# Optimization experiments

Measured on AMD Instinct MI355X. Metric: run time of the kernel, lower is better.

The kernel has to match this reference:

```python
import jax, jax.numpy as jnp
import numpy as np

B, S, D = 4, 2048, 512
H, DK, DV = 8, 64, 64


def setup_inputs() -> dict:
    key = jax.random.key(0)
    ks = jax.random.split(key, 12)
    inv = 1.0 / np.sqrt(D)
    return {
        "query": jax.random.normal(ks[0], (B, S, D), dtype=jnp.float32),
        "value": jax.random.normal(ks[1], (B, S, D), dtype=jnp.float32),
        "attention_mask": jax.random.randint(ks[2], (B, S), 0, 2, dtype=jnp.int32),
        "Wq": jax.random.normal(ks[3], (D, H * DK), dtype=jnp.float32) * inv,
        "bq": jnp.zeros((H * DK,), dtype=jnp.float32),
        "Wk": jax.random.normal(ks[4], (D, H * DK), dtype=jnp.float32) * inv,
        "bk": jnp.zeros((H * DK,), dtype=jnp.float32),
        "Wv": jax.random.normal(ks[5], (D, H * DV), dtype=jnp.float32) * inv,
        "bv": jnp.zeros((H * DV,), dtype=jnp.float32),
        "Wo": jax.random.normal(ks[6], (H * DV, D), dtype=jnp.float32) * inv,
        "bo": jnp.zeros((D,), dtype=jnp.float32),
    }


def _split_heads(x, h):
    b, s, _ = x.shape
    return x.reshape(b, s, h, -1).transpose(0, 2, 1, 3)  # (B,H,S,dh)


def reference(query, value, attention_mask, Wq, bq, Wk, bk, Wv, bv, Wo, bo):
    # QKV projections (activation=None -> identity); key defaults to value
    q = _split_heads(query @ Wq + bq, H)   # (B,H,S,DK)
    k = _split_heads(value @ Wk + bk, H)   # (B,H,S,DK)
    v = _split_heads(value @ Wv + bv, H)   # (B,H,S,DV)

    scores = jnp.einsum("bhqd,bhkd->bhqk", q, k) / jnp.sqrt(jnp.float32(DK))
    # additive mask: m = 1e9*(mask-1), applied on both key and query axes
    m = 1e9 * (attention_mask.astype(jnp.float32) - 1.0)  # (B,S)
    scores = scores + m[:, None, None, :] + m[:, None, :, None]

    weights = jax.nn.softmax(scores, axis=-1)
    ctx = jnp.einsum("bhqk,bhkd->bhqd", weights, v)        # (B,H,S,DV)
    ctx = ctx.transpose(0, 2, 1, 3).reshape(ctx.shape[0], ctx.shape[2], H * DV)
    return ctx @ Wo + bo  # (B,S,D)
```

## Files before the change

### kernel.cpp

```cpp
#include <hip/hip_runtime.h>

#define B_ 4
#define S_ 2048
#define D_ 512
#define H_ 8

typedef __attribute__((ext_vector_type(8))) __bf16 bf16x8;
typedef __attribute__((ext_vector_type(4))) float f32x4;

#define NEGBIG  -1.442695040e9f
#define QSCALE  0.18033688011112042f

__device__ __forceinline__ unsigned pack_rn(float a, float b) {
    union { float f; unsigned u; } ua, ub; ua.f = a; ub.f = b;
    return __builtin_amdgcn_perm(ub.u + 0x8000u, ua.u + 0x8000u, 0x07060302u);
}

__device__ __forceinline__ void gl16(const void* g, void* l) {
    __builtin_amdgcn_global_load_lds(
        (const __attribute__((address_space(1))) unsigned int*)g,
        (__attribute__((address_space(3))) unsigned int*)l, 16, 0, 0);
}

__global__ __launch_bounds__(256) void pre_all(
    const float* __restrict__ q, const float* __restrict__ v,
    const int* __restrict__ am,
    const float* __restrict__ Wq, const float* __restrict__ Wk,
    const float* __restrict__ Wv, const float* __restrict__ Wo,
    unsigned short* __restrict__ xq, unsigned short* __restrict__ xv,
    unsigned short* __restrict__ Tq, unsigned short* __restrict__ Tk,
    unsigned short* __restrict__ Tv, unsigned short* __restrict__ To,
    int* __restrict__ idxc, int* __restrict__ nvout,
    float* __restrict__ Mf, float* __restrict__ Mc)
{
    const int bid = blockIdx.x;
    const int tid = threadIdx.x;

    if (bid < 4096) {
        const int z = bid >> 11, xb = bid & 2047;
        const float* src = z ? v : q;
        unsigned short* dst = z ? xv : xq;
        int i = (xb * 256 + tid) * 8;
        float4 f0 = *(const float4*)&src[i];
        float4 f1 = *(const float4*)&src[i + 4];
        uint4 o;
        o.x = pack_rn(f0.x, f0.y); o.y = pack_rn(f0.z, f0.w);
        o.z = pack_rn(f1.x, f1.y); o.w = pack_rn(f1.z, f1.w);
        *(uint4*)&dst[i] = o;
    } else if (bid < 4352) {
        int r = bid - 4096;
        int z = r >> 6, rem = r & 63;
        const float* W = (z == 0) ? Wq : (z == 1) ? Wk : (z == 2) ? Wv : Wo;
        unsigned short* T = (z == 0) ? Tq : (z == 1) ? Tk : (z == 2) ? Tv : To;
        int n0 = (rem & 7) * 64, k0 = (rem >> 3) * 64;

        __shared__ float Ts[64][69];
        #pragma unroll
        for (int it = 0; it < 4; it++) {
            int lin = tid + it * 256;
            int kr = lin >> 4, c4 = (lin & 15) * 4;
            float4 vv = *(const float4*)&W[(k0 + kr) * 512 + n0 + c4];
            Ts[kr][c4 + 0] = vv.x; Ts[kr][c4 + 1] = vv.y;
            Ts[kr][c4 + 2] = vv.z; Ts[kr][c4 + 3] = vv.w;
        }
        __syncthreads();
        int n = tid >> 2, kc = tid & 3;
        unsigned p[8];
        #pragma unroll
        for (int j = 0; j < 8; j++)
            p[j] = pack_rn(Ts[kc * 16 + 2 * j][n], Ts[kc * 16 + 2 * j + 1][n]);
        unsigned short* dst = &T[(n0 + n) * 512 + k0 + kc * 16];
        *(uint4*)dst       = *(uint4*)&p[0];
        *(uint4*)(dst + 8) = *(uint4*)&p[4];
    } else {
        const int w = tid >> 6, lane = tid & 63;
        const int* amb = am + w * 2048;
        int m[32];
        #pragma unroll
        for (int s = 0; s < 32; s++) m[s] = amb[s * 64 + lane];

        int* ib = idxc + w * 2048;
        const unsigned long long lt = (1ULL << lane) - 1ULL;
        int base = 0;
        #pragma unroll
        for (int s = 0; s < 32; s++) {
            unsigned long long bal = __ballot(m[s] != 0);
            if (m[s]) ib[base + __popcll(bal & lt)] = s * 64 + lane;
            base += __popcll(bal);
        }
        const int nv = base;
        for (int i = nv + lane; i < 2048; i += 64) ib[i] = 0;
        float* mfb = Mf + w * 2048;
        float* mcb = Mc + w * 2048;
        #pragma unroll
        for (int s = 0; s < 32; s++) {
            int i = s * 64 + lane;
            mfb[i] = m[s] ? 0.f : NEGBIG;
            mcb[i] = (i < nv) ? 0.f : NEGBIG;
        }
        if (lane == 0) nvout[w] = nv;
    }
}

__global__ __launch_bounds__(256) void proj_qkv_mfma(
    const unsigned short* __restrict__ Xq, const unsigned short* __restrict__ Xv,
    const unsigned short* __restrict__ Wtq, const unsigned short* __restrict__ Wtk,
    const unsigned short* __restrict__ Wtv,
    const float* __restrict__ bq, const float* __restrict__ bk,
    const float* __restrict__ bv,
    const int* __restrict__ idxc, const int* __restrict__ nv1,
    unsigned short* __restrict__ Qb, unsigned short* __restrict__ Kb,
    unsigned short* __restrict__ VtG)
{
    const int z = blockIdx.z;
    const unsigned short* A  = (z == 0) ? Wtq : (z == 1) ? Wtk : Xv;
    const unsigned short* Bm = (z == 0) ? Xq  : (z == 1) ? Xv  : Wtv;
    const float* bias        = (z == 0) ? bq  : (z == 1) ? bk  : bv;
    const int lin0 = blockIdx.y * 128 + blockIdx.x;
    const int m0 = (z < 2) ? blockIdx.y * 128 : (lin0 >> 3) * 128;
    const int n0 = (z < 2) ? blockIdx.x * 64  : (lin0 & 7) * 64;

    if (z == 1) {
        int bb = n0 >> 11, cap = (nv1[bb] + 63) & ~63;
        if (cap < 64) cap = 64;
        if ((n0 & 2047) >= cap) return;
    }
    if (z == 2) {
        int bb = m0 >> 11, cap = (nv1[bb] + 63) & ~63;
        if (cap < 64) cap = 64;
        if ((m0 & 2047) >= cap) return;
    }

    const int tid = threadIdx.x;
    const int w = tid >> 6, lane = tid & 63;
    const int l15 = lane & 15, quad = lane >> 4;
    const int wm = (w >> 1) * 64, wn = (w & 1) * 32;

    __shared__ unsigned short As[2][128 * 64];
    __shared__ unsigned short Bs[2][64 * 64];

    const int srw  = tid >> 3;
    const int csrc = (tid & 7) ^ (srw & 7);
    const unsigned short* aS[4];
    const unsigned short* bS[2];
    #pragma unroll
    for (int is = 0; is < 4; is++) {
        int ra = m0 + is * 32 + srw;
        long sa = ra;
        if (z == 2) { int bb = ra >> 11; sa = (long)bb * 2048 + idxc[bb * 2048 + (ra & 2047)]; }
        aS[is] = A + sa * 512 + csrc * 8;
    }
    #pragma unroll
    for (int is = 0; is < 2; is++) {
        int rb = n0 + is * 32 + srw;
        long sb = rb;
        if (z == 1) { int bb = rb >> 11; sb = (long)bb * 2048 + idxc[bb * 2048 + (rb & 2047)]; }
        bS[is] = Bm + sb * 512 + csrc * 8;
    }

    const int koff0 = ((quad    ) ^ (l15 & 7)) * 8;
    const int koff1 = ((quad + 4) ^ (l15 & 7)) * 8;

    f32x4 acc[4][2];
    #pragma unroll
    for (int i = 0; i < 4; i++)
        #pragma unroll
        for (int j = 0; j < 2; j++) acc[i][j] = (f32x4){0.f, 0.f, 0.f, 0.f};

    #define STAGE_Q(buf, k0)                                        \
        do {                                                        \
            _Pragma("unroll")                                       \
            for (int is = 0; is < 4; is++)                          \
                gl16(aS[is] + (k0), &As[buf][is * 2048 + w * 512]); \
            _Pragma("unroll")                                       \
            for (int is = 0; is < 2; is++)                          \
                gl16(bS[is] + (k0), &Bs[buf][is * 2048 + w * 512]); \
        } while (0)

    STAGE_Q(0, 0);
    for (int k = 0; k < 8; k++) {
        const int cur = k & 1;
        if (k < 7) {
            STAGE_Q(cur ^ 1, (k + 1) * 64);
            asm volatile("s_waitcnt vmcnt(6)" ::: "memory");
        } else {
            asm volatile("s_waitcnt vmcnt(0)" ::: "memory");
        }
        asm volatile("s_barrier" ::: "memory");
        #pragma unroll
        for (int kc = 0; kc < 2; kc++) {
            const int ko = kc ? koff1 : koff0;
            bf16x8 a[4], bb[2];
            #pragma unroll
            for (int i = 0; i < 4; i++)
                a[i] = *(const bf16x8*)&As[cur][(wm + 16 * i + l15) * 64 + ko];
            #pragma unroll
            for (int j = 0; j < 2; j++)
                bb[j] = *(const bf16x8*)&Bs[cur][(wn + 16 * j + l15) * 64 + ko];
            #pragma unroll
            for (int i = 0; i < 4; i++)
                #pragma unroll
                for (int j = 0; j < 2; j++)
                    acc[i][j] = __builtin_amdgcn_mfma_f32_16x16x32_bf16(a[i], bb[j], acc[i][j], 0, 0, 0);
        }
        asm volatile("s_barrier" ::: "memory");
    }
    #undef STAGE_Q

    if (z == 2) {
        #pragma unroll
        for (int j = 0; j < 2; j++) {
            int N = n0 + wn + 16 * j + l15;
            float bv_ = bias[N];
            int h = N >> 6, d = N & 63;
            #pragma unroll
            for (int i = 0; i < 4; i++) {
                int Mb = m0 + wm + 16 * i + quad * 4;
                int b = Mb >> 11, s = Mb & 2047;
                uint2 o;
                o.x = pack_rn(acc[i][j][0] + bv_, acc[i][j][1] + bv_);
                o.y = pack_rn(acc[i][j][2] + bv_, acc[i][j][3] + bv_);
                *(uint2*)&VtG[((b * H_ + h) * 64 + d) * 2048 + s] = o;
            }
        }
    } else {
        unsigned short* dst = (z == 0) ? Qb : Kb;
        const float scale = (z == 0) ? QSCALE : 1.0f;
        #pragma unroll
        for (int j = 0; j < 2; j++) {
            int sg = n0 + wn + 16 * j + l15;
            int b = sg >> 11, s = sg & 2047;
            #pragma unroll
            for (int i = 0; i < 4; i++) {
                int F = m0 + wm + 16 * i + quad * 4;
                int h = F >> 6, d = F & 63;
                float4 b4 = *(const float4*)&bias[F];
                uint2 o;
                o.x = pack_rn((acc[i][j][0] + b4.x) * scale, (acc[i][j][1] + b4.y) * scale);
                o.y = pack_rn((acc[i][j][2] + b4.z) * scale, (acc[i][j][3] + b4.w) * scale);
                *(uint2*)&dst[((b * H_ + h) * 2048 + s) * 64 + d] = o;
            }
        }
    }
}

__global__ __launch_bounds__(256, 2) void flash_mfma(
    const unsigned short* __restrict__ Qg, const unsigned short* __restrict__ Kg,
    const unsigned short* __restrict__ VtG, const float* __restrict__ Mf,
    const float* __restrict__ Mc, const int* __restrict__ nvalid,
    unsigned short* __restrict__ ctxB)
{
    const int bid = blockIdx.x;
    const int xcd = bid & 7, idx = bid >> 3;
    const int bh = xcd * 4 + (idx & 3);
    const int q0 = (idx >> 2) * 128;
    const int b = bh >> 3, h = bh & 7;

    const int tid = threadIdx.x;
    const int w = tid >> 6, lane = tid & 63;
    const int l15 = lane & 15, quad = lane >> 4;
    const int swz = l15 & 7;

    __shared__ unsigned short Ks[2][64 * 64];
    __shared__ unsigned short Ps[4][32 * 64];
    unsigned short* pw = &Ps[w][0];

    const int nv = nvalid[b];
    int ntiles = (nv + 63) >> 6;
    if (ntiles < 1) ntiles = 1;

    const float* mfb = Mf + b * 2048;
    const float* mcp = Mc + b * 2048 + quad * 4;

    bf16x8 qf[2][2];
    float mq[2];
    #pragma unroll
    for (int qb = 0; qb < 2; qb++) {
        int qrow = q0 + w * 32 + qb * 16 + l15;
        const unsigned short* p = &Qg[((long)bh * 2048 + qrow) * 64 + quad * 8];
        qf[qb][0] = *(const bf16x8*)p;
        qf[qb][1] = *(const bf16x8*)(p + 32);
        mq[qb] = mfb[qrow];
    }

    const unsigned short* vp[4];
    #pragma unroll
    for (int i = 0; i < 4; i++)
        vp[i] = VtG + ((long)bh * 64 + i * 16 + l15) * 2048 + quad * 8;

    const int srow = tid >> 2;
    const int sch  = (tid & 3) * 2;
    const unsigned short* kgb = Kg + (long)bh * 2048 * 64;
    const int sw0 = srow * 64 + ((sch    ) ^ (srow & 7)) * 8;
    const int sw1 = srow * 64 + ((sch + 1) ^ (srow & 7)) * 8;

    {
        uint4 a = *(const uint4*)&kgb[srow * 64 + sch * 8];
        uint4 c = *(const uint4*)&kgb[srow * 64 + sch * 8 + 8];
        *(uint4*)&Ks[0][sw0] = a;
        *(uint4*)&Ks[0][sw1] = c;
    }

    const int koff0 = ((quad    ) ^ swz) * 8;
    const int koff1 = ((quad + 4) ^ swz) * 8;

    f32x4 accO[2][4];
    #pragma unroll
    for (int qb = 0; qb < 2; qb++)
        #pragma unroll
        for (int dt = 0; dt < 4; dt++) accO[qb][dt] = (f32x4){0.f, 0.f, 0.f, 0.f};
    float mi[2] = {-3.0e38f, -3.0e38f};
    float li[2] = {0.f, 0.f};

    __syncthreads();

    for (int t = 0; t < ntiles; t++) {
        const int kt = t * 64;
        const int ktn = (t + 1 < ntiles) ? kt + 64 : kt;
        const int cur = t & 1, nxt = cur ^ 1;

        bf16x8 vf[4][2];
        #pragma unroll
        for (int dt = 0; dt < 4; dt++) {
            vf[dt][0] = *(const bf16x8*)(vp[dt] + kt);
            vf[dt][1] = *(const bf16x8*)(vp[dt] + kt + 32);
        }
        uint4 kst0 = *(const uint4*)&kgb[(ktn + srow) * 64 + sch * 8];
        uint4 kst1 = *(const uint4*)&kgb[(ktn + srow) * 64 + sch * 8 + 8];
        f32x4 kmf[4];
        #pragma unroll
        for (int nt = 0; nt < 4; nt++)
            kmf[nt] = *(const f32x4*)(mcp + kt + nt * 16);

        bf16x8 kf[4][2];
        #pragma unroll
        for (int nt = 0; nt < 4; nt++) {
            kf[nt][0] = *(const bf16x8*)&Ks[cur][(nt * 16 + l15) * 64 + koff0];
            kf[nt][1] = *(const bf16x8*)&Ks[cur][(nt * 16 + l15) * 64 + koff1];
        }
        f32x4 sc[2][4];
        #pragma unroll
        for (int qb = 0; qb < 2; qb++)
            #pragma unroll
            for (int nt = 0; nt < 4; nt++) {
                f32x4 c = kmf[nt];
                c[0] += mq[qb]; c[1] += mq[qb]; c[2] += mq[qb]; c[3] += mq[qb];
                sc[qb][nt] = c;
            }
        __builtin_amdgcn_s_setprio(1);
        #pragma unroll
        for (int qb = 0; qb < 2; qb++)
            #pragma unroll
            for (int nt = 0; nt < 4; nt++) {
                sc[qb][nt] = __builtin_amdgcn_mfma_f32_16x16x32_bf16(
                    kf[nt][0], qf[qb][0], sc[qb][nt], 0, 0, 0);
                sc[qb][nt] = __builtin_amdgcn_mfma_f32_16x16x32_bf16(
                    kf[nt][1], qf[qb][1], sc[qb][nt], 0, 0, 0);
            }
        __builtin_amdgcn_s_setprio(0);

        #pragma unroll
        for (int qb = 0; qb < 2; qb++) {
            float mloc = fmaxf(fmaxf(sc[qb][0][0], sc[qb][0][1]),
                               fmaxf(sc[qb][0][2], sc[qb][0][3]));
            #pragma unroll
            for (int nt = 1; nt < 4; nt++)
                mloc = fmaxf(mloc, fmaxf(fmaxf(sc[qb][nt][0], sc[qb][nt][1]),
                                         fmaxf(sc[qb][nt][2], sc[qb][nt][3])));
            mloc = fmaxf(mloc, __shfl_xor(mloc, 16));
            mloc = fmaxf(mloc, __shfl_xor(mloc, 32));

            float mn = mi[qb];
            if (!__all(mloc <= mn + 4.f)) {
                float mo = mn;
                mn = fmaxf(mo, mloc);
                float alpha = __builtin_amdgcn_exp2f(mo - mn);
                li[qb] *= alpha;
                #pragma unroll
                for (int dt = 0; dt < 4; dt++) {
                    accO[qb][dt][0] *= alpha; accO[qb][dt][1] *= alpha;
                    accO[qb][dt][2] *= alpha; accO[qb][dt][3] *= alpha;
                }
                mi[qb] = mn;
            }

            float ps = 0.f;
            const int prbase = (qb * 16 + l15) * 64;
            #pragma unroll
            for (int nt = 0; nt < 4; nt++) {
                float p0 = __builtin_amdgcn_exp2f(sc[qb][nt][0] - mn);
                float p1 = __builtin_amdgcn_exp2f(sc[qb][nt][1] - mn);
                float p2 = __builtin_amdgcn_exp2f(sc[qb][nt][2] - mn);
                float p3 = __builtin_amdgcn_exp2f(sc[qb][nt][3] - mn);
                ps += (p0 + p1) + (p2 + p3);
                uint2 pp;
                pp.x = pack_rn(p0, p1);
                pp.y = pack_rn(p2, p3);
                *(uint2*)&pw[prbase + ((2 * nt + (quad >> 1)) ^ swz) * 8 + (quad & 1) * 4] = pp;
            }
            ps += __shfl_xor(ps, 16);
            ps += __shfl_xor(ps, 32);
            li[qb] += ps;
        }

        #pragma unroll
        for (int qb = 0; qb < 2; qb++) {
            bf16x8 pf0 = *(const bf16x8*)&pw[(qb * 16 + l15) * 64 + koff0];
            bf16x8 pf1 = *(const bf16x8*)&pw[(qb * 16 + l15) * 64 + koff1];
            __builtin_amdgcn_s_setprio(1);
            #pragma unroll
            for (int dt = 0; dt < 4; dt++) {
                accO[qb][dt] = __builtin_amdgcn_mfma_f32_16x16x32_bf16(
                    vf[dt][0], pf0, accO[qb][dt], 0, 0, 0);
                accO[qb][dt] = __builtin_amdgcn_mfma_f32_16x16x32_bf16(
                    vf[dt][1], pf1, accO[qb][dt], 0, 0, 0);
            }
            __builtin_amdgcn_s_setprio(0);
        }

        *(uint4*)&Ks[nxt][sw0] = kst0;
        *(uint4*)&Ks[nxt][sw1] = kst1;
        __syncthreads();
    }

    #pragma unroll
    for (int qb = 0; qb < 2; qb++) {
        float inv = 1.f / li[qb];
        int q = q0 + w * 32 + qb * 16 + l15;
        int obase = (b * 2048 + q) * 512 + h * 64 + quad * 4;
        #pragma unroll
        for (int dt = 0; dt < 4; dt++) {
            uint2 o;
            o.x = pack_rn(accO[qb][dt][0] * inv, accO[qb][dt][1] * inv);
            o.y = pack_rn(accO[qb][dt][2] * inv, accO[qb][dt][3] * inv);
            *(uint2*)&ctxB[obase + dt * 16] = o;
        }
    }
}

__global__ __launch_bounds__(256) void proj_out_mfma(
    const unsigned short* __restrict__ ctxB, const unsigned short* __restrict__ Wto,
    const float* __restrict__ bo, float* __restrict__ out)
{
    const int m0 = blockIdx.y * 128, n0 = blockIdx.x * 64;
    const int tid = threadIdx.x;
    const int w = tid >> 6, lane = tid & 63;
    const int l15 = lane & 15, quad = lane >> 4;
    const int wm = (w >> 1) * 64, wn = (w & 1) * 32;

    __shared__ unsigned short As[2][128 * 64];
    __shared__ unsigned short Bs[2][64 * 64];

    const int srw  = tid >> 3;
    const int csrc = (tid & 7) ^ (srw & 7);
    const unsigned short* aS[4];
    const unsigned short* bS[2];
    #pragma unroll
    for (int is = 0; is < 4; is++)
        aS[is] = Wto  + (long)(m0 + is * 32 + srw) * 512 + csrc * 8;
    #pragma unroll
    for (int is = 0; is < 2; is++)
        bS[is] = ctxB + (long)(n0 + is * 32 + srw) * 512 + csrc * 8;

    const int koff0 = ((quad    ) ^ (l15 & 7)) * 8;
    const int koff1 = ((quad + 4) ^ (l15 & 7)) * 8;

    f32x4 acc[4][2];
    #pragma unroll
    for (int i = 0; i < 4; i++)
        #pragma unroll
        for (int j = 0; j < 2; j++) acc[i][j] = (f32x4){0.f, 0.f, 0.f, 0.f};

    #define STAGE_O(buf, k0)                                        \
        do {                                                        \
            _Pragma("unroll")                                       \
            for (int is = 0; is < 4; is++)                          \
                gl16(aS[is] + (k0), &As[buf][is * 2048 + w * 512]); \
            _Pragma("unroll")                                       \
            for (int is = 0; is < 2; is++)                          \
                gl16(bS[is] + (k0), &Bs[buf][is * 2048 + w * 512]); \
        } while (0)

    STAGE_O(0, 0);
    for (int k = 0; k < 8; k++) {
        const int cur = k & 1;
        if (k < 7) {
            STAGE_O(cur ^ 1, (k + 1) * 64);
            asm volatile("s_waitcnt vmcnt(6)" ::: "memory");
        } else {
            asm volatile("s_waitcnt vmcnt(0)" ::: "memory");
        }
        asm volatile("s_barrier" ::: "memory");
        #pragma unroll
        for (int kc = 0; kc < 2; kc++) {
            const int ko = kc ? koff1 : koff0;
            bf16x8 a[4], bb[2];
            #pragma unroll
            for (int i = 0; i < 4; i++)
                a[i] = *(const bf16x8*)&As[cur][(wm + 16 * i + l15) * 64 + ko];
            #pragma unroll
            for (int j = 0; j < 2; j++)
                bb[j] = *(const bf16x8*)&Bs[cur][(wn + 16 * j + l15) * 64 + ko];
            #pragma unroll
            for (int i = 0; i < 4; i++)
                #pragma unroll
                for (int j = 0; j < 2; j++)
                    acc[i][j] = __builtin_amdgcn_mfma_f32_16x16x32_bf16(a[i], bb[j], acc[i][j], 0, 0, 0);
        }
        asm volatile("s_barrier" ::: "memory");
    }
    #undef STAGE_O

    #pragma unroll
    for (int j = 0; j < 2; j++) {
        int sg = n0 + wn + 16 * j + l15;
        #pragma unroll
        for (int i = 0; i < 4; i++) {
            int F = m0 + wm + 16 * i + quad * 4;
            float4 b4 = *(const float4*)&bo[F];
            float4 vv;
            vv.x = acc[i][j][0] + b4.x;
            vv.y = acc[i][j][1] + b4.y;
            vv.z = acc[i][j][2] + b4.z;
            vv.w = acc[i][j][3] + b4.w;
            *(float4*)&out[sg * 512 + F] = vv;
        }
    }
}

extern "C" void kernel_launch(void* const* d_in, const int* in_sizes, int n_in,
                              void* d_out, int out_size, void* d_ws, size_t ws_size,
                              hipStream_t stream)
{
    const float* query = (const float*)d_in[0];
    const float* value = (const float*)d_in[1];
    const int*   amask = (const int*)d_in[2];
    const float* Wq = (const float*)d_in[3];
    const float* bq = (const float*)d_in[4];
    const float* Wk = (const float*)d_in[5];
    const float* bk = (const float*)d_in[6];
    const float* Wv = (const float*)d_in[7];
    const float* bv = (const float*)d_in[8];
    const float* Wo = (const float*)d_in[9];
    const float* bo = (const float*)d_in[10];
    float* out = (float*)d_out;

    char* ws = (char*)d_ws;
    const size_t MB = 1 << 20;
    const size_t KB = 1 << 10;
    unsigned short* Xbq = (unsigned short*)(ws);
    unsigned short* Xbv = (unsigned short*)(ws + 8 * MB);
    unsigned short* Wtq = (unsigned short*)(ws + 16 * MB);
    unsigned short* Wtk = (unsigned short*)(ws + 16 * MB + MB / 2);
    unsigned short* Wtv = (unsigned short*)(ws + 17 * MB);
    unsigned short* Wto = (unsigned short*)(ws + 17 * MB + MB / 2);
    unsigned short* Qb  = (unsigned short*)(ws + 18 * MB);
    unsigned short* Kb  = (unsigned short*)(ws + 26 * MB);
    unsigned short* VtG = (unsigned short*)(ws + 34 * MB);
    int*   idx1 = (int*)(ws + 42 * MB);
    float* Mf   = (float*)(ws + 42 * MB + 32 * KB);
    float* Mc   = (float*)(ws + 42 * MB + 64 * KB);
    int*   nv   = (int*)(ws + 42 * MB + 96 * KB);
    unsigned short* ctx = Xbq;

    pre_all<<<dim3(4353), 256, 0, stream>>>(query, value, amask,
                                            Wq, Wk, Wv, Wo,
                                            Xbq, Xbv, Wtq, Wtk, Wtv, Wto,
                                            idx1, nv, Mf, Mc);
    proj_qkv_mfma<<<dim3(128, 4, 3), 256, 0, stream>>>(Xbq, Xbv, Wtq, Wtk, Wtv,
                                                       bq, bk, bv, idx1, nv,
                                                       Qb, Kb, VtG);
    flash_mfma<<<dim3(512), 256, 0, stream>>>(Qb, Kb, VtG, Mf, Mc, nv, ctx);
    proj_out_mfma<<<dim3(128, 4), 256, 0, stream>>>(ctx, Wto, bo, out);
}
```

Before: 182.8 us.

## Double flash-attention key tile from 64 to 128 keys per iteration

Each loop iteration of the flash attention kernel now covers 128 keys instead of 64. The K staging, P buffer, score tiles and PV MFMA chains are all enlarged, and the second half of V is loaded after the QK MFMAs. This halves the loop trips, barriers and online-softmax max/rescale steps per key, at the cost of more registers and LDS (32 KB Ks plus 32 KB Ps). The larger footprint may hurt the two-blocks-per-CU occupancy, and padding for nvalid now rounds up to 128.

```diff
diff --git a/kernel.cpp b/kernel.cpp
--- a/kernel.cpp
+++ b/kernel.cpp
@@ -261,12 +261,12 @@
     const int l15 = lane & 15, quad = lane >> 4;
     const int swz = l15 & 7;
 
-    __shared__ unsigned short Ks[2][64 * 64];
-    __shared__ unsigned short Ps[4][32 * 64];
+    __shared__ unsigned short Ks[2][128 * 64];
+    __shared__ unsigned short Ps[4][32 * 128];
     unsigned short* pw = &Ps[w][0];
 
     const int nv = nvalid[b];
-    int ntiles = (nv + 63) >> 6;
+    int ntiles = (nv + 127) >> 7;
     if (ntiles < 1) ntiles = 1;
 
     const float* mfb = Mf + b * 2048;
@@ -288,18 +288,17 @@
     for (int i = 0; i < 4; i++)
         vp[i] = VtG + ((long)bh * 64 + i * 16 + l15) * 2048 + quad * 8;
 
-    const int srow = tid >> 2;
-    const int sch  = (tid & 3) * 2;
+    const int srow = tid >> 1;
+    const int sch  = (tid & 1) * 4;
     const unsigned short* kgb = Kg + (long)bh * 2048 * 64;
-    const int sw0 = srow * 64 + ((sch    ) ^ (srow & 7)) * 8;
-    const int sw1 = srow * 64 + ((sch + 1) ^ (srow & 7)) * 8;
-
-    {
-        uint4 a = *(const uint4*)&kgb[srow * 64 + sch * 8];
-        uint4 c = *(const uint4*)&kgb[srow * 64 + sch * 8 + 8];
-        *(uint4*)&Ks[0][sw0] = a;
-        *(uint4*)&Ks[0][sw1] = c;
-    }
+    int swk[4];
+    #pragma unroll
+    for (int j = 0; j < 4; j++)
+        swk[j] = srow * 64 + ((sch + j) ^ (srow & 7)) * 8;
+
+    #pragma unroll
+    for (int j = 0; j < 4; j++)
+        *(uint4*)&Ks[0][swk[j]] = *(const uint4*)&kgb[srow * 64 + (sch + j) * 8];
 
     const int koff0 = ((quad    ) ^ swz) * 8;
     const int koff1 = ((quad + 4) ^ swz) * 8;
@@ -315,56 +314,61 @@
     __syncthreads();
 
     for (int t = 0; t < ntiles; t++) {
-        const int kt = t * 64;
-        const int ktn = (t + 1 < ntiles) ? kt + 64 : kt;
+        const int kt = t * 128;
+        const int ktn = (t + 1 < ntiles) ? kt + 128 : kt;
         const int cur = t & 1, nxt = cur ^ 1;
 
-        bf16x8 vf[4][2];
+        bf16x8 vfA[4][2], vfB[4][2];
         #pragma unroll
         for (int dt = 0; dt < 4; dt++) {
-            vf[dt][0] = *(const bf16x8*)(vp[dt] + kt);
-            vf[dt][1] = *(const bf16x8*)(vp[dt] + kt + 32);
-        }
-        uint4 kst0 = *(const uint4*)&kgb[(ktn + srow) * 64 + sch * 8];
-        uint4 kst1 = *(const uint4*)&kgb[(ktn + srow) * 64 + sch * 8 + 8];
-        f32x4 kmf[4];
-        #pragma unroll
-        for (int nt = 0; nt < 4; nt++)
+            vfA[dt][0] = *(const bf16x8*)(vp[dt] + kt);
+            vfA[dt][1] = *(const bf16x8*)(vp[dt] + kt + 32);
+        }
+        uint4 kst[4];
+        #pragma unroll
+        for (int j = 0; j < 4; j++)
+            kst[j] = *(const uint4*)&kgb[(ktn + srow) * 64 + (sch + j) * 8];
+        f32x4 kmf[8];
+        #pragma unroll
+        for (int nt = 0; nt < 8; nt++)
             kmf[nt] = *(const f32x4*)(mcp + kt + nt * 16);
 
-        bf16x8 kf[4][2];
-        #pragma unroll
-        for (int nt = 0; nt < 4; nt++) {
-            kf[nt][0] = *(const bf16x8*)&Ks[cur][(nt * 16 + l15) * 64 + koff0];
-            kf[nt][1] = *(const bf16x8*)&Ks[cur][(nt * 16 + l15) * 64 + koff1];
-        }
-        f32x4 sc[2][4];
+        f32x4 sc[2][8];
         #pragma unroll
         for (int qb = 0; qb < 2; qb++)
             #pragma unroll
-            for (int nt = 0; nt < 4; nt++) {
+            for (int nt = 0; nt < 8; nt++) {
                 f32x4 c = kmf[nt];
                 c[0] += mq[qb]; c[1] += mq[qb]; c[2] += mq[qb]; c[3] += mq[qb];
                 sc[qb][nt] = c;
             }
         __builtin_amdgcn_s_setprio(1);
         #pragma unroll
-        for (int qb = 0; qb < 2; qb++)
-            #pragma unroll
-            for (int nt = 0; nt < 4; nt++) {
+        for (int nt = 0; nt < 8; nt++) {
+            bf16x8 kf0 = *(const bf16x8*)&Ks[cur][(nt * 16 + l15) * 64 + koff0];
+            bf16x8 kf1 = *(const bf16x8*)&Ks[cur][(nt * 16 + l15) * 64 + koff1];
+            #pragma unroll
+            for (int qb = 0; qb < 2; qb++) {
                 sc[qb][nt] = __builtin_amdgcn_mfma_f32_16x16x32_bf16(
-                    kf[nt][0], qf[qb][0], sc[qb][nt], 0, 0, 0);
+                    kf0, qf[qb][0], sc[qb][nt], 0, 0, 0);
                 sc[qb][nt] = __builtin_amdgcn_mfma_f32_16x16x32_bf16(
-                    kf[nt][1], qf[qb][1], sc[qb][nt], 0, 0, 0);
-            }
+                    kf1, qf[qb][1], sc[qb][nt], 0, 0, 0);
+            }
+        }
         __builtin_amdgcn_s_setprio(0);
+
+        #pragma unroll
+        for (int dt = 0; dt < 4; dt++) {
+            vfB[dt][0] = *(const bf16x8*)(vp[dt] + kt + 64);
+            vfB[dt][1] = *(const bf16x8*)(vp[dt] + kt + 96);
+        }
 
         #pragma unroll
         for (int qb = 0; qb < 2; qb++) {
             float mloc = fmaxf(fmaxf(sc[qb][0][0], sc[qb][0][1]),
                                fmaxf(sc[qb][0][2], sc[qb][0][3]));
             #pragma unroll
-            for (int nt = 1; nt < 4; nt++)
+            for (int nt = 1; nt < 8; nt++)
                 mloc = fmaxf(mloc, fmaxf(fmaxf(sc[qb][nt][0], sc[qb][nt][1]),
                                          fmaxf(sc[qb][nt][2], sc[qb][nt][3])));
             mloc = fmaxf(mloc, __shfl_xor(mloc, 16));
@@ -385,9 +389,9 @@
             }
 
             float ps = 0.f;
-            const int prbase = (qb * 16 + l15) * 64;
-            #pragma unroll
-            for (int nt = 0; nt < 4; nt++) {
+            const int prbase = (qb * 16 + l15) * 128;
+            #pragma unroll
+            for (int nt = 0; nt < 8; nt++) {
                 float p0 = __builtin_amdgcn_exp2f(sc[qb][nt][0] - mn);
                 float p1 = __builtin_amdgcn_exp2f(sc[qb][nt][1] - mn);
                 float p2 = __builtin_amdgcn_exp2f(sc[qb][nt][2] - mn);
@@ -405,21 +409,28 @@
 
         #pragma unroll
         for (int qb = 0; qb < 2; qb++) {
-            bf16x8 pf0 = *(const bf16x8*)&pw[(qb * 16 + l15) * 64 + koff0];
-            bf16x8 pf1 = *(const bf16x8*)&pw[(qb * 16 + l15) * 64 + koff1];
+            bf16x8 pf[4];
+            #pragma unroll
+            for (int kc = 0; kc < 4; kc++)
+                pf[kc] = *(const bf16x8*)&pw[(qb * 16 + l15) * 128 + ((quad + 4 * kc) ^ swz) * 8];
             __builtin_amdgcn_s_setprio(1);
             #pragma unroll
             for (int dt = 0; dt < 4; dt++) {
                 accO[qb][dt] = __builtin_amdgcn_mfma_f32_16x16x32_bf16(
-                    vf[dt][0], pf0, accO[qb][dt], 0, 0, 0);
+                    vfA[dt][0], pf[0], accO[qb][dt], 0, 0, 0);
                 accO[qb][dt] = __builtin_amdgcn_mfma_f32_16x16x32_bf16(
-                    vf[dt][1], pf1, accO[qb][dt], 0, 0, 0);
+                    vfA[dt][1], pf[1], accO[qb][dt], 0, 0, 0);
+                accO[qb][dt] = __builtin_amdgcn_mfma_f32_16x16x32_bf16(
+                    vfB[dt][0], pf[2], accO[qb][dt], 0, 0, 0);
+                accO[qb][dt] = __builtin_amdgcn_mfma_f32_16x16x32_bf16(
+                    vfB[dt][1], pf[3], accO[qb][dt], 0, 0, 0);
             }
             __builtin_amdgcn_s_setprio(0);
         }
 
-        *(uint4*)&Ks[nxt][sw0] = kst0;
-        *(uint4*)&Ks[nxt][sw1] = kst1;
+        #pragma unroll
+        for (int j = 0; j < 4; j++)
+            *(uint4*)&Ks[nxt][swk[j]] = kst[j];
         __syncthreads();
     }
 
```

New measurement: 186.8 us. +2.2%, slower.

## Software-pipeline QK^T MFMA of next tile with softmax of current tile

Applied to the files above, without the earlier changes.

Restructures the attention loop so each step computes the score MFMAs for tile t+1 while running softmax and PV for tile t. Score buffers ping-pong between two register arrays, and K staging now runs two tiles ahead, with the LDS store and barrier moved before the next tile's score computation. The aim is to hide MFMA latency behind exp/reduction ALU work and to keep global K loads further in flight. In exchange it raises register pressure with a second score array, which could lower occupancy. On the last tile it also reads the mask array 64 elements past the current tile, a value that is never used.

```diff
diff --git a/kernel.cpp b/kernel.cpp
--- a/kernel.cpp
+++ b/kernel.cpp
@@ -300,6 +300,9 @@
         *(uint4*)&Ks[0][sw0] = a;
         *(uint4*)&Ks[0][sw1] = c;
     }
+    const int kt1 = (ntiles > 1) ? 64 : 0;
+    uint4 kstA = *(const uint4*)&kgb[(kt1 + srow) * 64 + sch * 8];
+    uint4 kstB = *(const uint4*)&kgb[(kt1 + srow) * 64 + sch * 8 + 8];
 
     const int koff0 = ((quad    ) ^ swz) * 8;
     const int koff1 = ((quad + 4) ^ swz) * 8;
@@ -314,10 +317,35 @@
 
     __syncthreads();
 
-    for (int t = 0; t < ntiles; t++) {
+    f32x4 scA[2][4], scB[2][4];
+    {
+        f32x4 kmf[4];
+        #pragma unroll
+        for (int nt = 0; nt < 4; nt++)
+            kmf[nt] = *(const f32x4*)(mcp + nt * 16);
+        bf16x8 kf[4][2];
+        #pragma unroll
+        for (int nt = 0; nt < 4; nt++) {
+            kf[nt][0] = *(const bf16x8*)&Ks[0][(nt * 16 + l15) * 64 + koff0];
+            kf[nt][1] = *(const bf16x8*)&Ks[0][(nt * 16 + l15) * 64 + koff1];
+        }
+        #pragma unroll
+        for (int qb = 0; qb < 2; qb++)
+            #pragma unroll
+            for (int nt = 0; nt < 4; nt++) {
+                f32x4 c = kmf[nt];
+                c[0] += mq[qb]; c[1] += mq[qb]; c[2] += mq[qb]; c[3] += mq[qb];
+                c = __builtin_amdgcn_mfma_f32_16x16x32_bf16(kf[nt][0], qf[qb][0], c, 0, 0, 0);
+                c = __builtin_amdgcn_mfma_f32_16x16x32_bf16(kf[nt][1], qf[qb][1], c, 0, 0, 0);
+                scA[qb][nt] = c;
+            }
+    }
+
+    auto STEP = [&](f32x4 (&scCur)[2][4], f32x4 (&scNxt)[2][4], int t) {
         const int kt = t * 64;
-        const int ktn = (t + 1 < ntiles) ? kt + 64 : kt;
-        const int cur = t & 1, nxt = cur ^ 1;
+        const int n = (t & 1) ^ 1;
+        const bool hasNext = (t + 1 < ntiles);
+        const int kt2 = (t + 2 < ntiles) ? (t + 2) * 64 : (ntiles - 1) * 64;
 
         bf16x8 vf[4][2];
         #pragma unroll
@@ -325,48 +353,45 @@
             vf[dt][0] = *(const bf16x8*)(vp[dt] + kt);
             vf[dt][1] = *(const bf16x8*)(vp[dt] + kt + 32);
         }
-        uint4 kst0 = *(const uint4*)&kgb[(ktn + srow) * 64 + sch * 8];
-        uint4 kst1 = *(const uint4*)&kgb[(ktn + srow) * 64 + sch * 8 + 8];
+        uint4 k2A = *(const uint4*)&kgb[(kt2 + srow) * 64 + sch * 8];
+        uint4 k2B = *(const uint4*)&kgb[(kt2 + srow) * 64 + sch * 8 + 8];
         f32x4 kmf[4];
         #pragma unroll
         for (int nt = 0; nt < 4; nt++)
-            kmf[nt] = *(const f32x4*)(mcp + kt + nt * 16);
-
-        bf16x8 kf[4][2];
-        #pragma unroll
-        for (int nt = 0; nt < 4; nt++) {
-            kf[nt][0] = *(const bf16x8*)&Ks[cur][(nt * 16 + l15) * 64 + koff0];
-            kf[nt][1] = *(const bf16x8*)&Ks[cur][(nt * 16 + l15) * 64 + koff1];
-        }
-        f32x4 sc[2][4];
-        #pragma unroll
-        for (int qb = 0; qb < 2; qb++)
+            kmf[nt] = *(const f32x4*)(mcp + kt + 64 + nt * 16);
+
+        *(uint4*)&Ks[n][sw0] = kstA;
+        *(uint4*)&Ks[n][sw1] = kstB;
+        __syncthreads();
+        kstA = k2A; kstB = k2B;
+
+        if (hasNext) {
+            bf16x8 kf[4][2];
             #pragma unroll
             for (int nt = 0; nt < 4; nt++) {
-                f32x4 c = kmf[nt];
-                c[0] += mq[qb]; c[1] += mq[qb]; c[2] += mq[qb]; c[3] += mq[qb];
-                sc[qb][nt] = c;
+                kf[nt][0] = *(const bf16x8*)&Ks[n][(nt * 16 + l15) * 64 + koff0];
+                kf[nt][1] = *(const bf16x8*)&Ks[n][(nt * 16 + l15) * 64 + koff1];
             }
-        __builtin_amdgcn_s_setprio(1);
-        #pragma unroll
-        for (int qb = 0; qb < 2; qb++)
-            #pragma unroll
-            for (int nt = 0; nt < 4; nt++) {
-                sc[qb][nt] = __builtin_amdgcn_mfma_f32_16x16x32_bf16(
-                    kf[nt][0], qf[qb][0], sc[qb][nt], 0, 0, 0);
-                sc[qb][nt] = __builtin_amdgcn_mfma_f32_16x16x32_bf16(
-                    kf[nt][1], qf[qb][1], sc[qb][nt], 0, 0, 0);
-            }
-        __builtin_amdgcn_s_setprio(0);
+            #pragma unroll
+            for (int qb = 0; qb < 2; qb++)
+                #pragma unroll
+                for (int nt = 0; nt < 4; nt++) {
+                    f32x4 c = kmf[nt];
+                    c[0] += mq[qb]; c[1] += mq[qb]; c[2] += mq[qb]; c[3] += mq[qb];
+                    c = __builtin_amdgcn_mfma_f32_16x16x32_bf16(kf[nt][0], qf[qb][0], c, 0, 0, 0);
+                    c = __builtin_amdgcn_mfma_f32_16x16x32_bf16(kf[nt][1], qf[qb][1], c, 0, 0, 0);
+                    scNxt[qb][nt] = c;
+                }
+        }
 
         #pragma unroll
         for (int qb = 0; qb < 2; qb++) {
-            float mloc = fmaxf(fmaxf(sc[qb][0][0], sc[qb][0][1]),
-                               fmaxf(sc[qb][0][2], sc[qb][0][3]));
+            float mloc = fmaxf(fmaxf(scCur[qb][0][0], scCur[qb][0][1]),
+                               fmaxf(scCur[qb][0][2], scCur[qb][0][3]));
             #pragma unroll
             for (int nt = 1; nt < 4; nt++)
-                mloc = fmaxf(mloc, fmaxf(fmaxf(sc[qb][nt][0], sc[qb][nt][1]),
-                                         fmaxf(sc[qb][nt][2], sc[qb][nt][3])));
+                mloc = fmaxf(mloc, fmaxf(fmaxf(scCur[qb][nt][0], scCur[qb][nt][1]),
+                                         fmaxf(scCur[qb][nt][2], scCur[qb][nt][3])));
             mloc = fmaxf(mloc, __shfl_xor(mloc, 16));
             mloc = fmaxf(mloc, __shfl_xor(mloc, 32));
 
@@ -388,10 +413,10 @@
             const int prbase = (qb * 16 + l15) * 64;
             #pragma unroll
             for (int nt = 0; nt < 4; nt++) {
-                float p0 = __builtin_amdgcn_exp2f(sc[qb][nt][0] - mn);
-                float p1 = __builtin_amdgcn_exp2f(sc[qb][nt][1] - mn);
-                float p2 = __builtin_amdgcn_exp2f(sc[qb][nt][2] - mn);
-                float p3 = __builtin_amdgcn_exp2f(sc[qb][nt][3] - mn);
+                float p0 = __builtin_amdgcn_exp2f(scCur[qb][nt][0] - mn);
+                float p1 = __builtin_amdgcn_exp2f(scCur[qb][nt][1] - mn);
+                float p2 = __builtin_amdgcn_exp2f(scCur[qb][nt][2] - mn);
+                float p3 = __builtin_amdgcn_exp2f(scCur[qb][nt][3] - mn);
                 ps += (p0 + p1) + (p2 + p3);
                 uint2 pp;
                 pp.x = pack_rn(p0, p1);
@@ -417,10 +442,11 @@
             }
             __builtin_amdgcn_s_setprio(0);
         }
-
-        *(uint4*)&Ks[nxt][sw0] = kst0;
-        *(uint4*)&Ks[nxt][sw1] = kst1;
-        __syncthreads();
+    };
+
+    for (int t = 0; t < ntiles; t += 2) {
+        STEP(scA, scB, t);
+        if (t + 1 < ntiles) STEP(scB, scA, t + 1);
     }
 
     #pragma unroll
```

New measurement: 180.3 us. About the same (-1.3%).
